# Optimization experiments

Hardware: AMD Instinct MI355X
Metric: run time of the kernel (lower is better)

## Reference

```python
import jax, jax.numpy as jnp
import numpy as np

SIGMA_S = 1.0
SIGMA_R = 0.1
FR = int(np.ceil(3 * SIGMA_S))          # 3
K_SIZE = 2 * FR + 1                     # 7
B, C, H, W = 8, 3, 512, 512


def matlab_style_gauss2d(shape, sigma):
    m, n = [(ss - 1.0) / 2.0 for ss in shape]
    y, x = np.ogrid[-m:m + 1, -n:n + 1]
    h = np.exp(-(x * x + y * y) / (2.0 * sigma * sigma))
    h[h < np.finfo(h.dtype).eps * h.max()] = 0
    s = h.sum()
    if s != 0:
        h /= s
    return h.astype(np.float32)


GAUSS = matlab_style_gauss2d((K_SIZE, K_SIZE), SIGMA_S)  # [7,7]


def setup_inputs() -> dict:
    key = jax.random.key(0)
    x = jax.random.uniform(key, (B, C, H, W), dtype=jnp.float32)
    return {"input": x}


def reference(input) -> jnp.ndarray:
    # ReflectionPad2d(fr)
    padded = jnp.pad(input, ((0, 0), (0, 0), (FR, FR), (FR, FR)), mode="reflect")
    inv_2sr2 = 1.0 / (2.0 * SIGMA_R * SIGMA_R)
    loss_map = jnp.zeros_like(input)
    for k in range(K_SIZE):
        for l in range(K_SIZE):
            shifted = padded[:, :, k:k + H, l:l + W]            # [B,C,H,W]
            d = input - shifted
            # bilateral range weight * gaussian spatial weight (constant, as in
            # the original which stores weight_map as a raw non-grad tensor)
            w = jax.lax.stop_gradient(
                jnp.exp(-(d * d).sum(1, keepdims=True) * inv_2sr2) * GAUSS[k, l]
            )                                                    # [B,1,H,W]
            loss_map = loss_map + jnp.abs(d) * w
    return loss_map.mean()
```

## Files before the change

### kernel.cpp

```cpp
#include <hip/hip_runtime.h>

#define FR 3
#define KS 7
#define TLX 64
#define TLY 16
#define PPT 4
#define HX (TLX + 2*FR)
#define HY (TLY + FR)
#define LSTR 72
#define IMG_H 512
#define IMG_W 512
#define NB 8
#define NC 3
#define GXB (IMG_W / TLX)
#define GYB (IMG_H / TLY)
#define NMAIN (GXB * GYB * NB)
#define RIM_PER_IMG 6108
#define NRIM_THREADS (RIM_PER_IMG * NB)
#define NRIM_BLK ((NRIM_THREADS + 255) / 256)
#define NPART (NMAIN + NRIM_BLK)

#define KSC 8.493218f
#define K2F 72.134752f

constexpr double g1d[KS] = {0.011108996538242306, 0.1353352832366127,
                            0.6065306597126334,   1.0,
                            0.6065306597126334,   0.1353352832366127,
                            0.011108996538242306};
constexpr double SUMG = 1.0 + 2.0 * (0.011108996538242306 + 0.1353352832366127
                                     + 0.6065306597126334);
constexpr double INVN = 1.0 / (SUMG * SUMG);
constexpr double KD   = 8.493218;

__device__ __forceinline__ int refl(int i, int n) {
    i = (i < 0) ? -i : i;
    return (i >= n) ? (2*n - 2 - i) : i;
}

__global__ __launch_bounds__(256) void blt_main(const float* __restrict__ in,
                                                float* __restrict__ partial) {
    __shared__ float sm[NC][HY][LSTR];
    __shared__ float wsum[4];

    const int bx  = blockIdx.x * TLX;
    const int by  = blockIdx.y * TLY;
    const int b   = blockIdx.z;
    const int tx  = threadIdx.x;
    const int ty  = threadIdx.y;
    const int tid = ty * 64 + tx;
    const float* base = in + (size_t)b * NC * IMG_H * IMG_W;

    for (int idx = tid; idx < HY * HX; idx += 256) {
        int ly = idx / HX;
        int lx = idx - ly * HX;
        int gy = refl(by + ly - FR, IMG_H);
        int gx = refl(bx + lx - FR, IMG_W);
        #pragma unroll
        for (int c = 0; c < NC; ++c)
            sm[c][ly][lx] = base[(c * IMG_H + gy) * IMG_W + gx] * KSC;
    }
    __syncthreads();

    float glm[KS];
    #pragma unroll
    for (int l = 0; l < KS; ++l) {
        bool inx = (unsigned)(bx + tx + l - FR) < (unsigned)IMG_W;
        glm[l] = inx ? (float)(2.0 * g1d[l] * INVN / KD) : 0.0f;
    }

    const int r0 = ty * PPT;
    float gym[KS];
    #pragma unroll
    for (int rr = 0; rr < KS; ++rr)
        gym[rr] = (by + r0 + rr - FR >= 0) ? 1.0f : 0.0f;

    float c0[PPT], c1[PPT], c2[PPT], acc[PPT];
    #pragma unroll
    for (int i = 0; i < PPT; ++i) {
        c0[i] = sm[0][r0 + i + FR][tx + FR];
        c1[i] = sm[1][r0 + i + FR][tx + FR];
        c2[i] = sm[2][r0 + i + FR][tx + FR];
        acc[i] = 0.0f;
    }

    #pragma unroll
    for (int rr = 0; rr < KS; ++rr) {
        float v0[KS], v1[KS], v2[KS];
        #pragma unroll
        for (int l = 0; l < KS; ++l) {
            v0[l] = sm[0][r0 + rr][tx + l];
            v1[l] = sm[1][r0 + rr][tx + l];
            v2[l] = sm[2][r0 + rr][tx + l];
        }
        #pragma unroll
        for (int i = 0; i < PPT; ++i) {
            const int k = rr - i;
            if (k < 0 || k > FR) continue;
            const int lmax = (k == FR) ? FR : KS;
            float t = 0.0f;
            #pragma unroll
            for (int l = 0; l < 7; ++l) {
                if (l >= lmax) continue;
                float d0 = c0[i] - v0[l];
                float d1 = c1[i] - v1[l];
                float d2 = c2[i] - v2[l];
                float s = d0 * d0;
                s = fmaf(d1, d1, s);
                s = fmaf(d2, d2, s);
                float e = __builtin_amdgcn_exp2f(-s);
                float sa = fabsf(d0) + fabsf(d1);
                sa += fabsf(d2);
                t = fmaf(sa, e * glm[l], t);
            }
            acc[i] = fmaf(t, (float)g1d[k] * gym[rr], acc[i]);
        }
    }

    float a = acc[0] + acc[1] + acc[2] + acc[3];
    #pragma unroll
    for (int off = 32; off > 0; off >>= 1)
        a += __shfl_down(a, off, 64);
    if ((tid & 63) == 0) wsum[tid >> 6] = a;
    __syncthreads();
    if (tid == 0) {
        int bid = blockIdx.x + GXB * (blockIdx.y + GYB * blockIdx.z);
        partial[bid] = wsum[0] + wsum[1] + wsum[2] + wsum[3];
    }
}

__global__ __launch_bounds__(256) void blt_rim(const float* __restrict__ in,
                                               float* __restrict__ partial) {
    __shared__ float wsum[4];
    const int tid = threadIdx.x;
    const int idx = blockIdx.x * 256 + tid;
    float a = 0.0f;
    if (idx < NRIM_THREADS) {
        const int b = idx / RIM_PER_IMG;
        int r = idx - b * RIM_PER_IMG;
        int y, x;
        if (r < 3 * IMG_W) { y = r >> 9; x = r & (IMG_W - 1); }
        else if (r < 6 * IMG_W) { r -= 3 * IMG_W; y = (IMG_H - 3) + (r >> 9); x = r & (IMG_W - 1); }
        else if (r < 6 * IMG_W + 3 * (IMG_H - 6)) { r -= 6 * IMG_W; y = 3 + r / 3; x = r - 3 * (r / 3); }
        else { r -= 6 * IMG_W + 3 * (IMG_H - 6); y = 3 + r / 3; x = (IMG_W - 3) + (r - 3 * (r / 3)); }

        const float* base = in + (size_t)b * NC * IMG_H * IMG_W;
        const float cc0 = base[(0 * IMG_H + y) * IMG_W + x];
        const float cc1 = base[(1 * IMG_H + y) * IMG_W + x];
        const float cc2 = base[(2 * IMG_H + y) * IMG_W + x];

        #pragma unroll
        for (int k = 0; k < KS; ++k) {
            #pragma unroll
            for (int l = 0; l < KS; ++l) {
                if (k == FR && l == FR) continue;
                const int dy = k - FR, dx = l - FR;
                int qy = y + dy, qx = x + dx;
                bool oob = ((unsigned)qy >= (unsigned)IMG_H) | ((unsigned)qx >= (unsigned)IMG_W);
                if (oob) {
                    int ry = refl(qy, IMG_H), rx = refl(qx, IMG_W);
                    float v0 = base[(0 * IMG_H + ry) * IMG_W + rx];
                    float v1 = base[(1 * IMG_H + ry) * IMG_W + rx];
                    float v2 = base[(2 * IMG_H + ry) * IMG_W + rx];
                    float d0 = cc0 - v0, d1 = cc1 - v1, d2 = cc2 - v2;
                    float s = d0 * d0;
                    s = fmaf(d1, d1, s);
                    s = fmaf(d2, d2, s);
                    float e = __builtin_amdgcn_exp2f(-(K2F * s));
                    float sa = fabsf(d0) + fabsf(d1) + fabsf(d2);
                    a = fmaf(sa, e * (float)(g1d[k] * g1d[l] * INVN), a);
                }
            }
        }
    }
    #pragma unroll
    for (int off = 32; off > 0; off >>= 1)
        a += __shfl_down(a, off, 64);
    if ((tid & 63) == 0) wsum[tid >> 6] = a;
    __syncthreads();
    if (tid == 0) partial[NMAIN + blockIdx.x] = wsum[0] + wsum[1] + wsum[2] + wsum[3];
}

__global__ __launch_bounds__(256) void finalize_kernel(const float* __restrict__ partial,
                                                       float* __restrict__ out) {
    __shared__ float wsum[4];
    const int tid = threadIdx.x;
    float a = 0.0f;
    for (int i = tid; i < NPART; i += 256) a += partial[i];
    #pragma unroll
    for (int off = 32; off > 0; off >>= 1)
        a += __shfl_down(a, off, 64);
    if ((tid & 63) == 0) wsum[tid >> 6] = a;
    __syncthreads();
    if (tid == 0)
        out[0] = (wsum[0] + wsum[1] + wsum[2] + wsum[3]) / (float)(NB * NC * IMG_H * IMG_W);
}

extern "C" void kernel_launch(void* const* d_in, const int* in_sizes, int n_in,
                              void* d_out, int out_size, void* d_ws, size_t ws_size,
                              hipStream_t stream) {
    const float* in = (const float*)d_in[0];
    float* out = (float*)d_out;
    float* ws  = (float*)d_ws;

    dim3 grid(GXB, GYB, NB);
    dim3 block(TLX, 256 / TLX);
    blt_main<<<grid, block, 0, stream>>>(in, ws);
    blt_rim<<<NRIM_BLK, 256, 0, stream>>>(in, ws);
    finalize_kernel<<<1, 256, 0, stream>>>(ws, out);
}
```

Baseline: 98.49 us.

## Fuse main and rim kernels and compute two pixels per thread

Merges the interior tile kernel and the border-rim kernel into a single launch, with blocks split by index, which removes one kernel launch and its tail. Tiles widen to 128 columns so each thread computes two adjacent pixels and reads each shared-memory row window once with float2 loads. Center values are now taken from the same loaded window instead of being read separately. This raises register use, which could lower occupancy, and the rim blocks still run an unneeded __syncthreads.

```diff
diff --git a/kernel.cpp b/kernel.cpp
--- a/kernel.cpp
+++ b/kernel.cpp
@@ -2,12 +2,13 @@
 
 #define FR 3
 #define KS 7
-#define TLX 64
+#define TLX 128
 #define TLY 16
 #define PPT 4
+#define PPX 2
 #define HX (TLX + 2*FR)
 #define HY (TLY + FR)
-#define LSTR 72
+#define LSTR 136
 #define IMG_H 512
 #define IMG_W 512
 #define NB 8
@@ -18,7 +19,8 @@
 #define RIM_PER_IMG 6108
 #define NRIM_THREADS (RIM_PER_IMG * NB)
 #define NRIM_BLK ((NRIM_THREADS + 255) / 256)
-#define NPART (NMAIN + NRIM_BLK)
+#define NBLK_A (NMAIN + NRIM_BLK)
+#define NPART NBLK_A
 
 #define KSC 8.493218f
 #define K2F 72.134752f
@@ -31,153 +33,159 @@
                                      + 0.6065306597126334);
 constexpr double INVN = 1.0 / (SUMG * SUMG);
 constexpr double KD   = 8.493218;
+constexpr double WPAIR = 2.0 * INVN / KD;
 
 __device__ __forceinline__ int refl(int i, int n) {
     i = (i < 0) ? -i : i;
     return (i >= n) ? (2*n - 2 - i) : i;
 }
 
-__global__ __launch_bounds__(256) void blt_main(const float* __restrict__ in,
-                                                float* __restrict__ partial) {
+__global__ __launch_bounds__(256) void blt_fused(const float* __restrict__ in,
+                                                 float* __restrict__ partial) {
     __shared__ float sm[NC][HY][LSTR];
     __shared__ float wsum[4];
-
-    const int bx  = blockIdx.x * TLX;
-    const int by  = blockIdx.y * TLY;
-    const int b   = blockIdx.z;
-    const int tx  = threadIdx.x;
-    const int ty  = threadIdx.y;
-    const int tid = ty * 64 + tx;
-    const float* base = in + (size_t)b * NC * IMG_H * IMG_W;
-
-    for (int idx = tid; idx < HY * HX; idx += 256) {
-        int ly = idx / HX;
-        int lx = idx - ly * HX;
-        int gy = refl(by + ly - FR, IMG_H);
-        int gx = refl(bx + lx - FR, IMG_W);
-        #pragma unroll
-        for (int c = 0; c < NC; ++c)
-            sm[c][ly][lx] = base[(c * IMG_H + gy) * IMG_W + gx] * KSC;
-    }
-    __syncthreads();
-
-    float glm[KS];
-    #pragma unroll
-    for (int l = 0; l < KS; ++l) {
-        bool inx = (unsigned)(bx + tx + l - FR) < (unsigned)IMG_W;
-        glm[l] = inx ? (float)(2.0 * g1d[l] * INVN / KD) : 0.0f;
-    }
-
-    const int r0 = ty * PPT;
-    float gym[KS];
-    #pragma unroll
-    for (int rr = 0; rr < KS; ++rr)
-        gym[rr] = (by + r0 + rr - FR >= 0) ? 1.0f : 0.0f;
-
-    float c0[PPT], c1[PPT], c2[PPT], acc[PPT];
-    #pragma unroll
-    for (int i = 0; i < PPT; ++i) {
-        c0[i] = sm[0][r0 + i + FR][tx + FR];
-        c1[i] = sm[1][r0 + i + FR][tx + FR];
-        c2[i] = sm[2][r0 + i + FR][tx + FR];
-        acc[i] = 0.0f;
-    }
-
-    #pragma unroll
-    for (int rr = 0; rr < KS; ++rr) {
-        float v0[KS], v1[KS], v2[KS];
+    const int tid = threadIdx.x;
+    float a = 0.0f;
+
+    if (blockIdx.x < NMAIN) {
+        const int bid = blockIdx.x;
+        const int b   = bid >> 7;
+        const int rem = bid & 127;
+        const int by  = (rem >> 2) * TLY;
+        const int bx  = (rem & 3) * TLX;
+        const int tx  = tid & 63;
+        const int ty  = tid >> 6;
+        const float* base = in + (size_t)b * NC * IMG_H * IMG_W;
+
+        for (int idx = tid; idx < HY * HX; idx += 256) {
+            int ly = idx / HX;
+            int lx = idx - ly * HX;
+            int gy = refl(by + ly - FR, IMG_H);
+            int gx = refl(bx + lx - FR, IMG_W);
+            #pragma unroll
+            for (int c = 0; c < NC; ++c)
+                sm[c][ly][lx] = base[(c * IMG_H + gy) * IMG_W + gx] * KSC;
+        }
+        __syncthreads();
+
+        const int x0 = bx + 2 * tx;
+        float glm0[KS], glm1[KS];
         #pragma unroll
         for (int l = 0; l < KS; ++l) {
-            v0[l] = sm[0][r0 + rr][tx + l];
-            v1[l] = sm[1][r0 + rr][tx + l];
-            v2[l] = sm[2][r0 + rr][tx + l];
-        }
+            glm0[l] = ((unsigned)(x0 + l - FR)     < (unsigned)IMG_W) ? (float)(g1d[l] * WPAIR) : 0.0f;
+            glm1[l] = ((unsigned)(x0 + 1 + l - FR) < (unsigned)IMG_W) ? (float)(g1d[l] * WPAIR) : 0.0f;
+        }
+
+        const int r0 = ty * PPT;
+        float cc0[PPT][PPX], cc1[PPT][PPX], cc2[PPT][PPX];
+        float acc0 = 0.0f, acc1 = 0.0f;
+
         #pragma unroll
-        for (int i = 0; i < PPT; ++i) {
-            const int k = rr - i;
-            if (k < 0 || k > FR) continue;
-            const int lmax = (k == FR) ? FR : KS;
-            float t = 0.0f;
-            #pragma unroll
-            for (int l = 0; l < 7; ++l) {
-                if (l >= lmax) continue;
-                float d0 = c0[i] - v0[l];
-                float d1 = c1[i] - v1[l];
-                float d2 = c2[i] - v2[l];
-                float s = d0 * d0;
-                s = fmaf(d1, d1, s);
-                s = fmaf(d2, d2, s);
-                float e = __builtin_amdgcn_exp2f(-s);
-                float sa = fabsf(d0) + fabsf(d1);
-                sa += fabsf(d2);
-                t = fmaf(sa, e * glm[l], t);
+        for (int rr = KS - 1; rr >= 0; --rr) {
+            float w0[8], w1[8], w2[8];
+            #pragma unroll
+            for (int j = 0; j < 4; ++j) {
+                float2 t0 = *reinterpret_cast<const float2*>(&sm[0][r0 + rr][2 * tx + 2 * j]);
+                float2 t1 = *reinterpret_cast<const float2*>(&sm[1][r0 + rr][2 * tx + 2 * j]);
+                float2 t2 = *reinterpret_cast<const float2*>(&sm[2][r0 + rr][2 * tx + 2 * j]);
+                w0[2*j] = t0.x; w0[2*j+1] = t0.y;
+                w1[2*j] = t1.x; w1[2*j+1] = t1.y;
+                w2[2*j] = t2.x; w2[2*j+1] = t2.y;
             }
-            acc[i] = fmaf(t, (float)g1d[k] * gym[rr], acc[i]);
-        }
+            #pragma unroll
+            for (int i = 0; i < PPT; ++i) {
+                const int k = rr - i;
+                if (k < 0 || k > FR) continue;
+                if (k == FR) {
+                    cc0[i][0] = w0[3]; cc0[i][1] = w0[4];
+                    cc1[i][0] = w1[3]; cc1[i][1] = w1[4];
+                    cc2[i][0] = w2[3]; cc2[i][1] = w2[4];
+                }
+                const int lmax = (k == FR) ? FR : KS;
+                const float rw = (by + r0 + i + k >= FR) ? (float)g1d[k] : 0.0f;
+                float t0 = 0.0f, t1 = 0.0f;
+                #pragma unroll
+                for (int l = 0; l < KS; ++l) {
+                    if (l >= lmax) continue;
+                    {
+                        float d0 = cc0[i][0] - w0[l];
+                        float d1 = cc1[i][0] - w1[l];
+                        float d2 = cc2[i][0] - w2[l];
+                        float s = d0 * d0;
+                        s = fmaf(d1, d1, s);
+                        s = fmaf(d2, d2, s);
+                        float e = __builtin_amdgcn_exp2f(-s);
+                        float sa = fabsf(d0) + fabsf(d1);
+                        sa += fabsf(d2);
+                        t0 = fmaf(sa, e * glm0[l], t0);
+                    }
+                    {
+                        float d0 = cc0[i][1] - w0[l + 1];
+                        float d1 = cc1[i][1] - w1[l + 1];
+                        float d2 = cc2[i][1] - w2[l + 1];
+                        float s = d0 * d0;
+                        s = fmaf(d1, d1, s);
+                        s = fmaf(d2, d2, s);
+                        float e = __builtin_amdgcn_exp2f(-s);
+                        float sa = fabsf(d0) + fabsf(d1);
+                        sa += fabsf(d2);
+                        t1 = fmaf(sa, e * glm1[l], t1);
+                    }
+                }
+                acc0 = fmaf(t0, rw, acc0);
+                acc1 = fmaf(t1, rw, acc1);
+            }
+        }
+        a = acc0 + acc1;
+    } else {
+        const int idx = (blockIdx.x - NMAIN) * 256 + tid;
+        if (idx < NRIM_THREADS) {
+            const int b = idx / RIM_PER_IMG;
+            int r = idx - b * RIM_PER_IMG;
+            int y, x;
+            if (r < 3 * IMG_W) { y = r >> 9; x = r & (IMG_W - 1); }
+            else if (r < 6 * IMG_W) { r -= 3 * IMG_W; y = (IMG_H - 3) + (r >> 9); x = r & (IMG_W - 1); }
+            else if (r < 6 * IMG_W + 3 * (IMG_H - 6)) { r -= 6 * IMG_W; y = 3 + r / 3; x = r - 3 * (r / 3); }
+            else { r -= 6 * IMG_W + 3 * (IMG_H - 6); y = 3 + r / 3; x = (IMG_W - 3) + (r - 3 * (r / 3)); }
+
+            const float* base = in + (size_t)b * NC * IMG_H * IMG_W;
+            const float cc0 = base[(0 * IMG_H + y) * IMG_W + x];
+            const float cc1 = base[(1 * IMG_H + y) * IMG_W + x];
+            const float cc2 = base[(2 * IMG_H + y) * IMG_W + x];
+
+            #pragma unroll
+            for (int k = 0; k < KS; ++k) {
+                #pragma unroll
+                for (int l = 0; l < KS; ++l) {
+                    if (k == FR && l == FR) continue;
+                    int qy = y + k - FR, qx = x + l - FR;
+                    bool oob = ((unsigned)qy >= (unsigned)IMG_H) | ((unsigned)qx >= (unsigned)IMG_W);
+                    if (oob) {
+                        int ry = refl(qy, IMG_H), rx = refl(qx, IMG_W);
+                        float v0 = base[(0 * IMG_H + ry) * IMG_W + rx];
+                        float v1 = base[(1 * IMG_H + ry) * IMG_W + rx];
+                        float v2 = base[(2 * IMG_H + ry) * IMG_W + rx];
+                        float d0 = cc0 - v0, d1 = cc1 - v1, d2 = cc2 - v2;
+                        float s = d0 * d0;
+                        s = fmaf(d1, d1, s);
+                        s = fmaf(d2, d2, s);
+                        float e = __builtin_amdgcn_exp2f(-(K2F * s));
+                        float sa = fabsf(d0) + fabsf(d1) + fabsf(d2);
+                        a = fmaf(sa, e * (float)(g1d[k] * g1d[l] * INVN), a);
+                    }
+                }
+            }
+        }
+        __syncthreads();
     }
 
-    float a = acc[0] + acc[1] + acc[2] + acc[3];
     #pragma unroll
     for (int off = 32; off > 0; off >>= 1)
         a += __shfl_down(a, off, 64);
     if ((tid & 63) == 0) wsum[tid >> 6] = a;
     __syncthreads();
-    if (tid == 0) {
-        int bid = blockIdx.x + GXB * (blockIdx.y + GYB * blockIdx.z);
-        partial[bid] = wsum[0] + wsum[1] + wsum[2] + wsum[3];
-    }
-}
-
-__global__ __launch_bounds__(256) void blt_rim(const float* __restrict__ in,
-                                               float* __restrict__ partial) {
-    __shared__ float wsum[4];
-    const int tid = threadIdx.x;
-    const int idx = blockIdx.x * 256 + tid;
-    float a = 0.0f;
-    if (idx < NRIM_THREADS) {
-        const int b = idx / RIM_PER_IMG;
-        int r = idx - b * RIM_PER_IMG;
-        int y, x;
-        if (r < 3 * IMG_W) { y = r >> 9; x = r & (IMG_W - 1); }
-        else if (r < 6 * IMG_W) { r -= 3 * IMG_W; y = (IMG_H - 3) + (r >> 9); x = r & (IMG_W - 1); }
-        else if (r < 6 * IMG_W + 3 * (IMG_H - 6)) { r -= 6 * IMG_W; y = 3 + r / 3; x = r - 3 * (r / 3); }
-        else { r -= 6 * IMG_W + 3 * (IMG_H - 6); y = 3 + r / 3; x = (IMG_W - 3) + (r - 3 * (r / 3)); }
-
-        const float* base = in + (size_t)b * NC * IMG_H * IMG_W;
-        const float cc0 = base[(0 * IMG_H + y) * IMG_W + x];
-        const float cc1 = base[(1 * IMG_H + y) * IMG_W + x];
-        const float cc2 = base[(2 * IMG_H + y) * IMG_W + x];
-
-        #pragma unroll
-        for (int k = 0; k < KS; ++k) {
-            #pragma unroll
-            for (int l = 0; l < KS; ++l) {
-                if (k == FR && l == FR) continue;
-                const int dy = k - FR, dx = l - FR;
-                int qy = y + dy, qx = x + dx;
-                bool oob = ((unsigned)qy >= (unsigned)IMG_H) | ((unsigned)qx >= (unsigned)IMG_W);
-                if (oob) {
-                    int ry = refl(qy, IMG_H), rx = refl(qx, IMG_W);
-                    float v0 = base[(0 * IMG_H + ry) * IMG_W + rx];
-                    float v1 = base[(1 * IMG_H + ry) * IMG_W + rx];
-                    float v2 = base[(2 * IMG_H + ry) * IMG_W + rx];
-                    float d0 = cc0 - v0, d1 = cc1 - v1, d2 = cc2 - v2;
-                    float s = d0 * d0;
-                    s = fmaf(d1, d1, s);
-                    s = fmaf(d2, d2, s);
-                    float e = __builtin_amdgcn_exp2f(-(K2F * s));
-                    float sa = fabsf(d0) + fabsf(d1) + fabsf(d2);
-                    a = fmaf(sa, e * (float)(g1d[k] * g1d[l] * INVN), a);
-                }
-            }
-        }
-    }
-    #pragma unroll
-    for (int off = 32; off > 0; off >>= 1)
-        a += __shfl_down(a, off, 64);
-    if ((tid & 63) == 0) wsum[tid >> 6] = a;
-    __syncthreads();
-    if (tid == 0) partial[NMAIN + blockIdx.x] = wsum[0] + wsum[1] + wsum[2] + wsum[3];
+    if (tid == 0)
+        partial[blockIdx.x] = wsum[0] + wsum[1] + wsum[2] + wsum[3];
 }
 
 __global__ __launch_bounds__(256) void finalize_kernel(const float* __restrict__ partial,
@@ -202,9 +210,6 @@
     float* out = (float*)d_out;
     float* ws  = (float*)d_ws;
 
-    dim3 grid(GXB, GYB, NB);
-    dim3 block(TLX, 256 / TLX);
-    blt_main<<<grid, block, 0, stream>>>(in, ws);
-    blt_rim<<<NRIM_BLK, 256, 0, stream>>>(in, ws);
+    blt_fused<<<NBLK_A, 256, 0, stream>>>(in, ws);
     finalize_kernel<<<1, 256, 0, stream>>>(ws, out);
 }
```

Measured after the change: 94.73 us. 3.8% less time.
